# Kernel optimization log

Measured on AMD Instinct MI355X. Metric: run time of the kernel, lower is better.

## Reference

```python
import jax, jax.numpy as jnp
import numpy as np


def setup_inputs() -> dict:
    key = jax.random.key(0)
    k1, k2, k3 = jax.random.split(key, 3)
    B, C, H, W = 64, 1024, 32, 32
    x = jax.random.normal(k1, (B, C, H, W), dtype=jnp.float32)
    # Conv2d(C, 1, kernel_size=1): weight [1, C, 1, 1] -> flatten to [C], bias [1] -> scalar
    bound = 1.0 / np.sqrt(C)
    attn_w = jax.random.uniform(k2, (C,), dtype=jnp.float32, minval=-bound, maxval=bound)
    attn_b = jax.random.uniform(k3, (), dtype=jnp.float32, minval=-bound, maxval=bound)
    return {"x": x, "attn_w": attn_w, "attn_b": attn_b}


def reference(x, attn_w, attn_b):
    B, C, H, W = x.shape
    # 1x1 conv producing one channel: score[b,h,w] = sum_c x[b,c,h,w]*w[c] + b
    scores = jnp.einsum('bchw,c->bhw', x, attn_w) + attn_b          # [B,H,W]
    attn = jax.nn.softmax(scores.reshape(B, -1), axis=-1)           # softmax over H*W
    attn = attn.reshape(B, H, W)
    # weighted sum pooling over spatial dims
    out = jnp.einsum('bchw,bhw->bc', x, attn)                       # [B,C]
    return out
```

## Files before the change

kernel.cpp:

```cpp
#include <hip/hip_runtime.h>

#define NB 64
#define NC 1024
#define NHW 1024

__device__ inline float wave_reduce_max(float v) {
    #pragma unroll
    for (int off = 32; off; off >>= 1) v = fmaxf(v, __shfl_xor(v, off));
    return v;
}
__device__ inline float wave_reduce_sum(float v) {
    #pragma unroll
    for (int off = 32; off; off >>= 1) v += __shfl_xor(v, off);
    return v;
}

__global__ __launch_bounds__(256) void scores_kernel(
        const float* __restrict__ x, const float* __restrict__ w,
        const float* __restrict__ bias, float* __restrict__ scores) {
    const int b  = blockIdx.x >> 2;
    const int hw = ((blockIdx.x & 3) << 8) + threadIdx.x;
    const float* xb = x + ((size_t)b * NC) * NHW + hw;
    float acc = 0.0f;
    #pragma unroll 16
    for (int c = 0; c < NC; ++c) {
        acc += xb[(size_t)c * NHW] * w[c];
    }
    scores[b * NHW + hw] = acc + bias[0];
}

__global__ __launch_bounds__(256) void softmax_kernel(float* __restrict__ scores) {
    __shared__ float redm[4];
    __shared__ float reds[4];
    const int tid  = threadIdx.x;
    const int wave = tid >> 6, lane = tid & 63;
    float4* row = reinterpret_cast<float4*>(scores + blockIdx.x * NHW);
    float4 v = row[tid];

    float m = fmaxf(fmaxf(v.x, v.y), fmaxf(v.z, v.w));
    m = wave_reduce_max(m);
    if (lane == 0) redm[wave] = m;
    __syncthreads();
    m = fmaxf(fmaxf(redm[0], redm[1]), fmaxf(redm[2], redm[3]));

    float4 e;
    e.x = __expf(v.x - m); e.y = __expf(v.y - m);
    e.z = __expf(v.z - m); e.w = __expf(v.w - m);
    float s = e.x + e.y + e.z + e.w;
    s = wave_reduce_sum(s);
    if (lane == 0) reds[wave] = s;
    __syncthreads();
    const float inv = 1.0f / (reds[0] + reds[1] + reds[2] + reds[3]);

    e.x *= inv; e.y *= inv; e.z *= inv; e.w *= inv;
    row[tid] = e;
}

__global__ __launch_bounds__(256) void pool_kernel(
        const float* __restrict__ x, const float* __restrict__ attn,
        float* __restrict__ out) {
    const int wave = threadIdx.x >> 6;
    const int lane = threadIdx.x & 63;
    const int out_idx = (blockIdx.x << 2) + wave;
    const int b = out_idx >> 10;
    const float4* xr = reinterpret_cast<const float4*>(x + (size_t)out_idx * NHW);
    const float4* ar = reinterpret_cast<const float4*>(attn + b * NHW);

    float acc = 0.0f;
    #pragma unroll
    for (int i = 0; i < 4; ++i) {
        const float4 xv = xr[(i << 6) + lane];
        const float4 av = ar[(i << 6) + lane];
        acc += xv.x * av.x + xv.y * av.y + xv.z * av.z + xv.w * av.w;
    }
    acc = wave_reduce_sum(acc);
    if (lane == 0) out[out_idx] = acc;
}

extern "C" void kernel_launch(void* const* d_in, const int* in_sizes, int n_in,
                              void* d_out, int out_size, void* d_ws, size_t ws_size,
                              hipStream_t stream) {
    const float* x    = (const float*)d_in[0];
    const float* w    = (const float*)d_in[1];
    const float* bias = (const float*)d_in[2];
    float* out    = (float*)d_out;
    float* scores = (float*)d_ws;

    scores_kernel <<<NB * (NHW / 256), 256, 0, stream>>>(x, w, bias, scores);
    softmax_kernel<<<NB,               256, 0, stream>>>(scores);
    pool_kernel   <<<(NB * NC) / 4,    256, 0, stream>>>(x, scores, out);
}
```

Baseline: 81.63 us.

## Fuse score, softmax and pooling into single-pass split-softmax with combine kernel

Replaces the three-kernel pipeline with a fused kernel. Each block loads a 16-position spatial tile for all channels into registers, computes local scores, a local max and a local exp-sum, and writes partial pooled sums per channel. A second kernel rescales the partials flash-style using the per-tile max and sum, then reduces them. The input x is now read once instead of twice, at the cost of a 16MB partial buffer written and reread. The bias is dropped because softmax is shift-invariant.

```diff
diff --git a/kernel.cpp b/kernel.cpp
--- a/kernel.cpp
+++ b/kernel.cpp
@@ -3,90 +3,137 @@
 #define NB 64
 #define NC 1024
 #define NHW 1024
+#define THW 16
+#define NT (NHW / THW)
+#define CPT 4
 
-__device__ inline float wave_reduce_max(float v) {
+__global__ __launch_bounds__(256) void fused_partial_kernel(
+        const float* __restrict__ x, const float* __restrict__ w,
+        float* __restrict__ partial, float* __restrict__ mz) {
+    __shared__ float red[4][THW];
+    __shared__ float pbuf[THW];
+
+    const int tid  = threadIdx.x;
+    const int wave = tid >> 6, lane = tid & 63;
+    const int bid  = blockIdx.x;
+    const int b    = bid >> 6;
+    const int hw0  = (bid & 63) * THW;
+    const int c0   = tid * CPT;
+
+    float4 xv[CPT][THW / 4];
     #pragma unroll
-    for (int off = 32; off; off >>= 1) v = fmaxf(v, __shfl_xor(v, off));
-    return v;
-}
-__device__ inline float wave_reduce_sum(float v) {
+    for (int j = 0; j < CPT; ++j) {
+        const float* row = x + ((size_t)(b * NC + c0 + j) * NHW + hw0);
+        #pragma unroll
+        for (int k = 0; k < THW / 4; ++k)
+            xv[j][k] = reinterpret_cast<const float4*>(row)[k];
+    }
+    float wj[CPT];
     #pragma unroll
-    for (int off = 32; off; off >>= 1) v += __shfl_xor(v, off);
-    return v;
+    for (int j = 0; j < CPT; ++j) wj[j] = w[c0 + j];
+
+    float sp[THW];
+    #pragma unroll
+    for (int k = 0; k < THW; ++k) sp[k] = 0.0f;
+    #pragma unroll
+    for (int j = 0; j < CPT; ++j) {
+        #pragma unroll
+        for (int k = 0; k < THW / 4; ++k) {
+            sp[4 * k + 0] += xv[j][k].x * wj[j];
+            sp[4 * k + 1] += xv[j][k].y * wj[j];
+            sp[4 * k + 2] += xv[j][k].z * wj[j];
+            sp[4 * k + 3] += xv[j][k].w * wj[j];
+        }
+    }
+    #pragma unroll
+    for (int k = 0; k < THW; ++k) {
+        #pragma unroll
+        for (int off = 32; off; off >>= 1)
+            sp[k] += __shfl_xor(sp[k], off);
+    }
+    if (lane == 0) {
+        #pragma unroll
+        for (int k = 0; k < THW; ++k) red[wave][k] = sp[k];
+    }
+    __syncthreads();
+
+    if (tid < THW) {
+        float s = red[0][tid] + red[1][tid] + red[2][tid] + red[3][tid];
+        float m = s;
+        #pragma unroll
+        for (int off = 8; off; off >>= 1) m = fmaxf(m, __shfl_xor(m, off, 16));
+        float e = __expf(s - m);
+        float z = e;
+        #pragma unroll
+        for (int off = 8; off; off >>= 1) z += __shfl_xor(z, off, 16);
+        pbuf[tid] = e;
+        if (tid == 0) {
+            mz[2 * bid]     = m;
+            mz[2 * bid + 1] = z;
+        }
+    }
+    __syncthreads();
+
+    float pb[THW];
+    #pragma unroll
+    for (int k = 0; k < THW; ++k) pb[k] = pbuf[k];
+
+    float4 o;
+    float a[CPT];
+    #pragma unroll
+    for (int j = 0; j < CPT; ++j) {
+        a[j] = 0.0f;
+        #pragma unroll
+        for (int k = 0; k < THW / 4; ++k) {
+            a[j] += xv[j][k].x * pb[4 * k + 0];
+            a[j] += xv[j][k].y * pb[4 * k + 1];
+            a[j] += xv[j][k].z * pb[4 * k + 2];
+            a[j] += xv[j][k].w * pb[4 * k + 3];
+        }
+    }
+    o.x = a[0]; o.y = a[1]; o.z = a[2]; o.w = a[3];
+    reinterpret_cast<float4*>(partial + (size_t)bid * NC + c0)[0] = o;
 }
 
-__global__ __launch_bounds__(256) void scores_kernel(
-        const float* __restrict__ x, const float* __restrict__ w,
-        const float* __restrict__ bias, float* __restrict__ scores) {
-    const int b  = blockIdx.x >> 2;
-    const int hw = ((blockIdx.x & 3) << 8) + threadIdx.x;
-    const float* xb = x + ((size_t)b * NC) * NHW + hw;
-    float acc = 0.0f;
-    #pragma unroll 16
-    for (int c = 0; c < NC; ++c) {
-        acc += xb[(size_t)c * NHW] * w[c];
+__global__ __launch_bounds__(256) void combine_kernel(
+        const float* __restrict__ partial, const float* __restrict__ mz,
+        float* __restrict__ out) {
+    __shared__ float scale[NT];
+    const int tid = threadIdx.x;
+    const int b   = blockIdx.x >> 2;
+    const int c   = ((blockIdx.x & 3) << 8) + tid;
+
+    if (tid < NT) {
+        const float m_t = mz[2 * (b * NT + tid)];
+        const float Z_t = mz[2 * (b * NT + tid) + 1];
+        float m = m_t;
+        #pragma unroll
+        for (int off = 32; off; off >>= 1) m = fmaxf(m, __shfl_xor(m, off));
+        const float ew = __expf(m_t - m);
+        float z = Z_t * ew;
+        #pragma unroll
+        for (int off = 32; off; off >>= 1) z += __shfl_xor(z, off);
+        scale[tid] = ew / z;
     }
-    scores[b * NHW + hw] = acc + bias[0];
-}
-
-__global__ __launch_bounds__(256) void softmax_kernel(float* __restrict__ scores) {
-    __shared__ float redm[4];
-    __shared__ float reds[4];
-    const int tid  = threadIdx.x;
-    const int wave = tid >> 6, lane = tid & 63;
-    float4* row = reinterpret_cast<float4*>(scores + blockIdx.x * NHW);
-    float4 v = row[tid];
-
-    float m = fmaxf(fmaxf(v.x, v.y), fmaxf(v.z, v.w));
-    m = wave_reduce_max(m);
-    if (lane == 0) redm[wave] = m;
     __syncthreads();
-    m = fmaxf(fmaxf(redm[0], redm[1]), fmaxf(redm[2], redm[3]));
-
-    float4 e;
-    e.x = __expf(v.x - m); e.y = __expf(v.y - m);
-    e.z = __expf(v.z - m); e.w = __expf(v.w - m);
-    float s = e.x + e.y + e.z + e.w;
-    s = wave_reduce_sum(s);
-    if (lane == 0) reds[wave] = s;
-    __syncthreads();
-    const float inv = 1.0f / (reds[0] + reds[1] + reds[2] + reds[3]);
-
-    e.x *= inv; e.y *= inv; e.z *= inv; e.w *= inv;
-    row[tid] = e;
-}
-
-__global__ __launch_bounds__(256) void pool_kernel(
-        const float* __restrict__ x, const float* __restrict__ attn,
-        float* __restrict__ out) {
-    const int wave = threadIdx.x >> 6;
-    const int lane = threadIdx.x & 63;
-    const int out_idx = (blockIdx.x << 2) + wave;
-    const int b = out_idx >> 10;
-    const float4* xr = reinterpret_cast<const float4*>(x + (size_t)out_idx * NHW);
-    const float4* ar = reinterpret_cast<const float4*>(attn + b * NHW);
 
     float acc = 0.0f;
-    #pragma unroll
-    for (int i = 0; i < 4; ++i) {
-        const float4 xv = xr[(i << 6) + lane];
-        const float4 av = ar[(i << 6) + lane];
-        acc += xv.x * av.x + xv.y * av.y + xv.z * av.z + xv.w * av.w;
-    }
-    acc = wave_reduce_sum(acc);
-    if (lane == 0) out[out_idx] = acc;
+    const float* p = partial + (size_t)b * NT * NC + c;
+    #pragma unroll 8
+    for (int t = 0; t < NT; ++t)
+        acc += p[(size_t)t * NC] * scale[t];
+    out[b * NC + c] = acc;
 }
 
 extern "C" void kernel_launch(void* const* d_in, const int* in_sizes, int n_in,
                               void* d_out, int out_size, void* d_ws, size_t ws_size,
                               hipStream_t stream) {
-    const float* x    = (const float*)d_in[0];
-    const float* w    = (const float*)d_in[1];
-    const float* bias = (const float*)d_in[2];
-    float* out    = (float*)d_out;
-    float* scores = (float*)d_ws;
+    const float* x = (const float*)d_in[0];
+    const float* w = (const float*)d_in[1];
+    float* out     = (float*)d_out;
+    float* partial = (float*)d_ws;
+    float* mz      = partial + (size_t)NB * NT * NC;
 
-    scores_kernel <<<NB * (NHW / 256), 256, 0, stream>>>(x, w, bias, scores);
-    softmax_kernel<<<NB,               256, 0, stream>>>(scores);
-    pool_kernel   <<<(NB * NC) / 4,    256, 0, stream>>>(x, scores, out);
+    fused_partial_kernel<<<NB * NT, 256, 0, stream>>>(x, w, partial, mz);
+    combine_kernel<<<NB * (NC / 256), 256, 0, stream>>>(partial, mz, out);
 }
```

After: 120.4 us. +47.5%, slower.

## Split channel reduction into chunked partial scores and reverse pool block order

Applied to the files above, without the earlier changes.

The score computation is split across 16 channel chunks per batch, so each block reduces 64 channels with float4 loads and writes partial sums, and the softmax kernel adds up the partials. This gives more parallelism and wider loads than the old per-thread 1024-channel loop. The pool kernel now walks blocks in reverse so that recently touched x data may still be in cache. The bias is dropped because softmax is shift-invariant, at the cost of extra partial-sum traffic through the workspace.

```diff
diff --git a/kernel.cpp b/kernel.cpp
--- a/kernel.cpp
+++ b/kernel.cpp
@@ -3,6 +3,8 @@
 #define NB 64
 #define NC 1024
 #define NHW 1024
+#define NCHUNK 16
+#define CCH 64
 
 __device__ inline float wave_reduce_max(float v) {
     #pragma unroll
@@ -15,56 +17,71 @@
     return v;
 }
 
-__global__ __launch_bounds__(256) void scores_kernel(
+__global__ __launch_bounds__(256) void scores_partial_kernel(
         const float* __restrict__ x, const float* __restrict__ w,
-        const float* __restrict__ bias, float* __restrict__ scores) {
-    const int b  = blockIdx.x >> 2;
-    const int hw = ((blockIdx.x & 3) << 8) + threadIdx.x;
-    const float* xb = x + ((size_t)b * NC) * NHW + hw;
-    float acc = 0.0f;
-    #pragma unroll 16
-    for (int c = 0; c < NC; ++c) {
-        acc += xb[(size_t)c * NHW] * w[c];
+        float* __restrict__ partials) {
+    const int tid   = threadIdx.x;
+    const int b     = blockIdx.x >> 4;
+    const int chunk = blockIdx.x & 15;
+    const int c0    = chunk * CCH;
+    const float* xb = x + ((size_t)(b * NC + c0)) * NHW + tid * 4;
+
+    float4 ps = {0.f, 0.f, 0.f, 0.f};
+    #pragma unroll 8
+    for (int k = 0; k < CCH; ++k) {
+        const float4 v = *reinterpret_cast<const float4*>(xb + (size_t)k * NHW);
+        const float wk = w[c0 + k];
+        ps.x += v.x * wk; ps.y += v.y * wk;
+        ps.z += v.z * wk; ps.w += v.w * wk;
     }
-    scores[b * NHW + hw] = acc + bias[0];
+    reinterpret_cast<float4*>(partials + (size_t)blockIdx.x * NHW)[tid] = ps;
 }
 
-__global__ __launch_bounds__(256) void softmax_kernel(float* __restrict__ scores) {
+__global__ __launch_bounds__(256) void softmax_kernel(
+        const float* __restrict__ partials, float* __restrict__ attn) {
     __shared__ float redm[4];
     __shared__ float reds[4];
     const int tid  = threadIdx.x;
     const int wave = tid >> 6, lane = tid & 63;
-    float4* row = reinterpret_cast<float4*>(scores + blockIdx.x * NHW);
-    float4 v = row[tid];
+    const int b    = blockIdx.x;
 
-    float m = fmaxf(fmaxf(v.x, v.y), fmaxf(v.z, v.w));
+    float4 s = {0.f, 0.f, 0.f, 0.f};
+    #pragma unroll
+    for (int i = 0; i < NCHUNK; ++i) {
+        const float4 p = reinterpret_cast<const float4*>(
+            partials + (size_t)(b * NCHUNK + i) * NHW)[tid];
+        s.x += p.x; s.y += p.y; s.z += p.z; s.w += p.w;
+    }
+
+    float m = fmaxf(fmaxf(s.x, s.y), fmaxf(s.z, s.w));
     m = wave_reduce_max(m);
     if (lane == 0) redm[wave] = m;
     __syncthreads();
     m = fmaxf(fmaxf(redm[0], redm[1]), fmaxf(redm[2], redm[3]));
 
     float4 e;
-    e.x = __expf(v.x - m); e.y = __expf(v.y - m);
-    e.z = __expf(v.z - m); e.w = __expf(v.w - m);
-    float s = e.x + e.y + e.z + e.w;
-    s = wave_reduce_sum(s);
-    if (lane == 0) reds[wave] = s;
+    e.x = __expf(s.x - m); e.y = __expf(s.y - m);
+    e.z = __expf(s.z - m); e.w = __expf(s.w - m);
+    float z = e.x + e.y + e.z + e.w;
+    z = wave_reduce_sum(z);
+    if (lane == 0) reds[wave] = z;
     __syncthreads();
     const float inv = 1.0f / (reds[0] + reds[1] + reds[2] + reds[3]);
 
     e.x *= inv; e.y *= inv; e.z *= inv; e.w *= inv;
-    row[tid] = e;
+    reinterpret_cast<float4*>(attn + (size_t)b * NHW)[tid] = e;
 }
 
 __global__ __launch_bounds__(256) void pool_kernel(
         const float* __restrict__ x, const float* __restrict__ attn,
         float* __restrict__ out) {
+    const int rbid = (NB * NC / 4 - 1) - blockIdx.x;
     const int wave = threadIdx.x >> 6;
     const int lane = threadIdx.x & 63;
-    const int out_idx = (blockIdx.x << 2) + wave;
+    const int out_idx = (rbid << 2) + wave;
     const int b = out_idx >> 10;
     const float4* xr = reinterpret_cast<const float4*>(x + (size_t)out_idx * NHW);
-    const float4* ar = reinterpret_cast<const float4*>(attn + b * NHW);
+    const float4* ar = reinterpret_cast<const float4*>(attn + (size_t)b * NHW);
 
     float acc = 0.0f;
     #pragma unroll
@@ -80,13 +97,13 @@
 extern "C" void kernel_launch(void* const* d_in, const int* in_sizes, int n_in,
                               void* d_out, int out_size, void* d_ws, size_t ws_size,
                               hipStream_t stream) {
-    const float* x    = (const float*)d_in[0];
-    const float* w    = (const float*)d_in[1];
-    const float* bias = (const float*)d_in[2];
-    float* out    = (float*)d_out;
-    float* scores = (float*)d_ws;
+    const float* x = (const float*)d_in[0];
+    const float* w = (const float*)d_in[1];
+    float* out      = (float*)d_out;
+    float* partials = (float*)d_ws;
+    float* attn     = partials + (size_t)NB * NCHUNK * NHW;
 
-    scores_kernel <<<NB * (NHW / 256), 256, 0, stream>>>(x, w, bias, scores);
-    softmax_kernel<<<NB,               256, 0, stream>>>(scores);
-    pool_kernel   <<<(NB * NC) / 4,    256, 0, stream>>>(x, scores, out);
+    scores_partial_kernel<<<NB * NCHUNK, 256, 0, stream>>>(x, w, partials);
+    softmax_kernel<<<NB, 256, 0, stream>>>(partials, attn);
+    pool_kernel<<<(NB * NC) / 4, 256, 0, stream>>>(x, attn, out);
 }
```

Result: slower. 85.14 us (+4.3%).
